# Kernel optimization log

Measured on AMD Instinct MI355X. Metric: run time of the kernel, lower is better.

The kernel has to match this reference:

```python
import jax, jax.numpy as jnp
import numpy as np

DIM = 384
DIM_HEAD = 32
HEADS = DIM // DIM_HEAD  # 12
INNER = HEADS * DIM_HEAD  # 384
WSZ = 8
WSZ2 = 8
SCALE = DIM_HEAD ** -0.5


def setup_inputs() -> dict:
    key = jax.random.key(0)
    k1, k2, k3, k4 = jax.random.split(key, 4)
    B, H, W = 32, 64, 64
    x = jax.random.normal(k1, (B, H, W, DIM), dtype=jnp.float32)
    # 1x1 convs == dense matrices over the channel dim
    w_qkv = jax.random.normal(k2, (DIM, 3 * INNER), dtype=jnp.float32) * (DIM ** -0.5)
    w_out = jax.random.normal(k3, (INNER, DIM), dtype=jnp.float32) * (INNER ** -0.5)
    b_out = jax.random.normal(k4, (DIM,), dtype=jnp.float32) * 0.02
    return {"x": x, "w_qkv": w_qkv, "w_out": w_out, "b_out": b_out}


def reference(x, w_qkv, w_out, b_out):
    B, H, W, D = x.shape
    nh, nw = H // WSZ, W // WSZ2
    S = WSZ * WSZ2  # tokens per window
    # 'short' attention: partition into non-overlapping wsz x wsz2 windows
    xw = (x.reshape(B, nh, WSZ, nw, WSZ2, D)
           .transpose(0, 1, 3, 2, 4, 5)
           .reshape(B * nh * nw, S, D))  # [N, S, D]
    qkv = xw @ w_qkv  # [N, S, 3*INNER] (1x1 conv, no bias)
    q, k, v = jnp.split(qkv, 3, axis=-1)
    def split_heads(t):
        N = t.shape[0]
        return t.reshape(N, S, HEADS, DIM_HEAD).transpose(0, 2, 1, 3)  # [N, h, S, d]
    q, k, v = map(split_heads, (q, k, v))
    sim = jnp.einsum('nhid,nhjd->nhij', q * SCALE, k)  # [N, h, S, S]
    attn = jax.nn.softmax(sim, axis=-1)
    out = jnp.einsum('nhij,nhjd->nhid', attn, v)  # [N, h, S, d]
    out = out.transpose(0, 2, 1, 3).reshape(-1, S, INNER)  # [N, S, INNER]
    out = out @ w_out + b_out  # 1x1 conv with bias -> [N, S, D]
    # undo windowing back to [B, H, W, D]
    out = (out.reshape(B, nh, nw, WSZ, WSZ2, D)
              .transpose(0, 1, 3, 2, 4, 5)
              .reshape(B, H, W, D))
    return out
```

## Files before the change

kernel.cpp:

```cpp
#include <hip/hip_runtime.h>

typedef _Float16 f16;
typedef _Float16 f16x4 __attribute__((ext_vector_type(4)));
typedef _Float16 f16x8 __attribute__((ext_vector_type(8)));
typedef float f32x4 __attribute__((ext_vector_type(4)));

#define MFMA_F16(A, B, C) __builtin_amdgcn_mfma_f32_16x16x32_f16(A, B, C, 0, 0, 0)
#define GLDS16(gp, lp)                                                        \
  __builtin_amdgcn_global_load_lds(                                           \
      (const __attribute__((address_space(1))) void*)(gp),                    \
      (__attribute__((address_space(3))) void*)(lp), 16, 0, 0)

static constexpr int ROWS = 32 * 64 * 64;
static constexpr float SCALE = 0.17677669529663687f;

static constexpr size_t WQKVT_OFF = 0;
static constexpr size_t WOUTT_OFF = (size_t)1152 * 384 * 2;
static constexpr size_t QKV_OFF   = WOUTT_OFF + (size_t)384 * 384 * 2;
static constexpr size_t WS_NEEDED = QKV_OFF + (size_t)ROWS * 1152 * 2;

__global__ __launch_bounds__(256) void k_prep(const float* __restrict__ wqkv,
                                              const float* __restrict__ wout,
                                              f16* __restrict__ wqkvT,
                                              f16* __restrict__ woutT) {
  int idx = blockIdx.x * 256 + threadIdx.x;
  if (idx < 1152 * 384) {
    int c = idx / 384, k = idx - c * 384;
    wqkvT[idx] = (f16)wqkv[k * 1152 + c];
  } else {
    int i = idx - 1152 * 384;
    if (i < 384 * 384) {
      int c = i / 384, k = i - c * 384;
      woutT[i] = (f16)wout[k * 384 + c];
    }
  }
}

__global__ __launch_bounds__(256) void k_cvt(const float* __restrict__ X,
                                             f16* __restrict__ Xh) {
  int idx = blockIdx.x * 256 + threadIdx.x;
#pragma unroll
  for (int i = 0; i < 12; ++i) {
    size_t j = (size_t)(idx + i * 1048576) * 4;
    float4 v = *(const float4*)&X[j];
    f16x4 h;
    h[0] = (f16)v.x; h[1] = (f16)v.y; h[2] = (f16)v.z; h[3] = (f16)v.w;
    *(f16x4*)&Xh[j] = h;
  }
}

__global__ __launch_bounds__(256, 2) void k_qkv(const f16* __restrict__ Xh,
                                                const f16* __restrict__ Wt,
                                                f16* __restrict__ qkv) {
  __shared__ __align__(16) f16 smem[4][128 * 64];

  const int tid = threadIdx.x;
  const int id = blockIdx.x;
  const int s = id & 7, t = id >> 3;
  const int n0 = (t % 9) * 128;
  const int m0 = (s * 128 + t / 9) * 128;

  const int lane = tid & 63, wave = tid >> 6;
  const int lane15 = lane & 15, quad = lane >> 4;
  const int wm = (wave >> 1) * 64, wn = (wave & 1) * 64;

  const int r8 = lane >> 3, g7 = lane & 7;
  const int sg = ((g7 ^ r8) << 3);
  const f16* asrc[4];
  const f16* bsrc[4];
#pragma unroll
  for (int l = 0; l < 4; ++l) {
    asrc[l] = Xh + (size_t)(m0 + (wave * 4 + l) * 8 + r8) * 384 + sg;
    bsrc[l] = Wt + (size_t)(n0 + (wave * 4 + l) * 8 + r8) * 384 + sg;
  }

#define STAGE(buf, ks)                                                      \
  do {                                                                      \
    _Pragma("unroll") for (int l = 0; l < 4; ++l)                           \
        GLDS16(asrc[l] + (ks), &smem[(buf)][(wave * 4 + l) * 512]);         \
    _Pragma("unroll") for (int l = 0; l < 4; ++l)                           \
        GLDS16(bsrc[l] + (ks), &smem[2 + (buf)][(wave * 4 + l) * 512]);     \
  } while (0)

#define LDSOFF(row, kk) ((row) * 64 + ((((kk) * 4 + quad) ^ ((row) & 7)) << 3))

  f32x4 acc[4][4] = {};

  STAGE(0, 0);
  __syncthreads();

#pragma unroll
  for (int ti = 0; ti < 6; ++ti) {
    const int cur = ti & 1;
    if (ti < 5) STAGE(cur ^ 1, (ti + 1) * 64);
    __builtin_amdgcn_sched_barrier(0);

#pragma unroll
    for (int kk = 0; kk < 2; ++kk) {
      f16x8 af[4], bf[4];
#pragma unroll
      for (int i = 0; i < 4; ++i)
        af[i] = *(const f16x8*)&smem[cur][LDSOFF(wm + i * 16 + lane15, kk)];
#pragma unroll
      for (int j = 0; j < 4; ++j)
        bf[j] = *(const f16x8*)&smem[2 + cur][LDSOFF(wn + j * 16 + lane15, kk)];
#pragma unroll
      for (int i = 0; i < 4; ++i)
#pragma unroll
        for (int j = 0; j < 4; ++j)
          acc[i][j] = MFMA_F16(af[i], bf[j], acc[i][j]);
    }

    __syncthreads();
  }
#undef STAGE
#undef LDSOFF

  f16* Cs = (f16*)smem;
#pragma unroll
  for (int i = 0; i < 4; ++i)
#pragma unroll
    for (int j = 0; j < 4; ++j)
#pragma unroll
      for (int v = 0; v < 4; ++v)
        Cs[(wm + i * 16 + quad * 4 + v) * 136 + wn + j * 16 + lane15] = (f16)acc[i][j][v];
  __syncthreads();
#pragma unroll
  for (int l = 0; l < 8; ++l) {
    int idx = l * 256 + tid;
    int row = idx >> 4, c8 = (idx & 15) * 8;
    *(f16x8*)&qkv[(size_t)(m0 + row) * 1152 + n0 + c8] = *(const f16x8*)&Cs[row * 136 + c8];
  }
}

__global__ __launch_bounds__(256) void k_attn(const f16* __restrict__ qkv,
                                              const f16* __restrict__ woutT,
                                              const float* __restrict__ b_out,
                                              float* __restrict__ out) {
  __shared__ f16 vt[32 * 72];
  __shared__ f16 Pw[4][16 * 72];
  __shared__ f16 ao[64 * 392];

  const int tid = threadIdx.x;
  const int lane = tid & 63, wave = tid >> 6;
  const int lane15 = lane & 15, quad = lane >> 4;

  const int blk = blockIdx.x;
  const int b = blk >> 6, rem = blk & 63, wh = rem >> 3, ww = rem & 7;
  const int base = b * 4096 + wh * 512 + ww * 8;

  const int tq = wave * 16 + lane15;
  const size_t rowq = (size_t)(base + (tq >> 3) * 64 + (tq & 7)) * 1152;
  size_t rowk[4];
#pragma unroll
  for (int tj = 0; tj < 4; ++tj) {
    int tk = tj * 16 + lane15;
    rowk[tj] = (size_t)(base + (tk >> 3) * 64 + (tk & 7)) * 1152;
  }
  const int vt_t = tid >> 2, vt_d8 = (tid & 3) * 8;
  const size_t rowv = (size_t)(base + (vt_t >> 3) * 64 + (vt_t & 7)) * 1152;

#pragma unroll 1
  for (int h = 0; h < 12; ++h) {
    const int hoff = h * 32;
    f16x8 vv = *(const f16x8*)&qkv[rowv + 768 + hoff + vt_d8];
#pragma unroll
    for (int j = 0; j < 8; ++j) vt[(vt_d8 + j) * 72 + vt_t] = vv[j];
    __syncthreads();

    f16x8 aq = *(const f16x8*)&qkv[rowq + hoff + quad * 8];
    f32x4 sim[4];
#pragma unroll
    for (int tj = 0; tj < 4; ++tj) {
      f16x8 bk = *(const f16x8*)&qkv[rowk[tj] + 384 + hoff + quad * 8];
      f32x4 z = {};
      sim[tj] = MFMA_F16(aq, bk, z);
    }
#pragma unroll
    for (int tj = 0; tj < 4; ++tj)
#pragma unroll
      for (int v = 0; v < 4; ++v) sim[tj][v] *= SCALE;

    float pv[4][4];
#pragma unroll
    for (int v = 0; v < 4; ++v) {
      float m = fmaxf(fmaxf(sim[0][v], sim[1][v]), fmaxf(sim[2][v], sim[3][v]));
#pragma unroll
      for (int off = 1; off < 16; off <<= 1) m = fmaxf(m, __shfl_xor(m, off));
      float ssum = 0.f;
#pragma unroll
      for (int tj = 0; tj < 4; ++tj) {
        pv[tj][v] = __expf(sim[tj][v] - m);
        ssum += pv[tj][v];
      }
#pragma unroll
      for (int off = 1; off < 16; off <<= 1) ssum += __shfl_xor(ssum, off);
      float inv = 1.0f / ssum;
#pragma unroll
      for (int tj = 0; tj < 4; ++tj) pv[tj][v] *= inv;
    }
#pragma unroll
    for (int tj = 0; tj < 4; ++tj)
#pragma unroll
      for (int v = 0; v < 4; ++v)
        Pw[wave][(quad * 4 + v) * 72 + tj * 16 + lane15] = (f16)pv[tj][v];
    __syncthreads();

    f32x4 o[2] = {};
#pragma unroll
    for (int kk = 0; kk < 64; kk += 32) {
      f16x8 pa = *(const f16x8*)&Pw[wave][lane15 * 72 + kk + quad * 8];
#pragma unroll
      for (int tj = 0; tj < 2; ++tj) {
        f16x8 bvv = *(const f16x8*)&vt[(tj * 16 + lane15) * 72 + kk + quad * 8];
        o[tj] = MFMA_F16(pa, bvv, o[tj]);
      }
    }
#pragma unroll
    for (int tj = 0; tj < 2; ++tj)
#pragma unroll
      for (int v = 0; v < 4; ++v)
        ao[(wave * 16 + quad * 4 + v) * 392 + hoff + tj * 16 + lane15] = (f16)o[tj][v];
    __syncthreads();
  }

  const int n0 = wave * 96;
  float biasv[6];
#pragma unroll
  for (int tj = 0; tj < 6; ++tj) biasv[tj] = b_out[n0 + tj * 16 + lane15];
  f32x4 acc[4][6] = {};
  for (int ksi = 0; ksi < 12; ++ksi) {
    const int ks = ksi * 32;
    f16x8 af[4];
#pragma unroll
    for (int ti = 0; ti < 4; ++ti)
      af[ti] = *(const f16x8*)&ao[(ti * 16 + lane15) * 392 + ks + quad * 8];
#pragma unroll
    for (int tj = 0; tj < 6; ++tj) {
      f16x8 bf = *(const f16x8*)&woutT[(size_t)(n0 + tj * 16 + lane15) * 384 + ks + quad * 8];
#pragma unroll
      for (int ti = 0; ti < 4; ++ti) acc[ti][tj] = MFMA_F16(af[ti], bf, acc[ti][tj]);
    }
  }
#pragma unroll
  for (int ti = 0; ti < 4; ++ti)
#pragma unroll
    for (int v = 0; v < 4; ++v) {
      int t = ti * 16 + quad * 4 + v;
      size_t row = (size_t)(base + (t >> 3) * 64 + (t & 7)) * 384;
#pragma unroll
      for (int tj = 0; tj < 6; ++tj)
        out[row + n0 + tj * 16 + lane15] = acc[ti][tj][v] + biasv[tj];
    }
}

extern "C" void kernel_launch(void* const* d_in, const int* in_sizes, int n_in,
                              void* d_out, int out_size, void* d_ws, size_t ws_size,
                              hipStream_t stream) {
  const float* x = (const float*)d_in[0];
  const float* w_qkv = (const float*)d_in[1];
  const float* w_out = (const float*)d_in[2];
  const float* b_out = (const float*)d_in[3];
  float* out = (float*)d_out;

  if (ws_size < WS_NEEDED) return;

  char* ws = (char*)d_ws;
  f16* wqkvT = (f16*)(ws + WQKVT_OFF);
  f16* woutT = (f16*)(ws + WOUTT_OFF);
  f16* qkv = (f16*)(ws + QKV_OFF);
  f16* Xh = (f16*)d_out;

  hipLaunchKernelGGL(k_prep, dim3(2304), dim3(256), 0, stream, w_qkv, w_out, wqkvT, woutT);
  hipLaunchKernelGGL(k_cvt, dim3(4096), dim3(256), 0, stream, x, Xh);
  hipLaunchKernelGGL(k_qkv, dim3(9216), dim3(256), 0, stream, Xh, wqkvT, qkv);
  hipLaunchKernelGGL(k_attn, dim3(2048), dim3(256), 0, stream, qkv, woutT, b_out, out);
}
```

Measured before the change: 753.8 us.

## Split attention and output projection; per-wave heads with in-place AO writeback

Attention now gives each wave its own heads, three per wave, and drops the block-wide barriers. The attention output is written back in place over the Q slots of the qkv buffer. The output projection moves to a separate tiled GEMM kernel with LDS double buffering and async global-to-LDS loads, sized 128x128 tiles. The softmax scale is folded into the Q weights during prep. This trades an extra round trip of the attention output through global memory for a much more efficient output GEMM and less synchronisation in attention.

```diff
diff --git a/kernel.cpp b/kernel.cpp
--- a/kernel.cpp
+++ b/kernel.cpp
@@ -26,7 +26,8 @@
   int idx = blockIdx.x * 256 + threadIdx.x;
   if (idx < 1152 * 384) {
     int c = idx / 384, k = idx - c * 384;
-    wqkvT[idx] = (f16)wqkv[k * 1152 + c];
+    float w = wqkv[k * 1152 + c];
+    wqkvT[idx] = (f16)(c < 384 ? w * SCALE : w);
   } else {
     int i = idx - 1152 * 384;
     if (i < 384 * 384) {
@@ -110,7 +111,6 @@
         for (int j = 0; j < 4; ++j)
           acc[i][j] = MFMA_F16(af[i], bf[j], acc[i][j]);
     }
-
     __syncthreads();
   }
 #undef STAGE
@@ -133,13 +133,9 @@
   }
 }
 
-__global__ __launch_bounds__(256) void k_attn(const f16* __restrict__ qkv,
-                                              const f16* __restrict__ woutT,
-                                              const float* __restrict__ b_out,
-                                              float* __restrict__ out) {
-  __shared__ f16 vt[32 * 72];
-  __shared__ f16 Pw[4][16 * 72];
-  __shared__ f16 ao[64 * 392];
+__global__ __launch_bounds__(256, 3) void k_attn(f16* __restrict__ qkv) {
+  __shared__ f16 vt[4][32 * 72];
+  __shared__ f16 Pt[4][16 * 72];
 
   const int tid = threadIdx.x;
   const int lane = tid & 63, wave = tid >> 6;
@@ -149,109 +145,177 @@
   const int b = blk >> 6, rem = blk & 63, wh = rem >> 3, ww = rem & 7;
   const int base = b * 4096 + wh * 512 + ww * 8;
 
-  const int tq = wave * 16 + lane15;
-  const size_t rowq = (size_t)(base + (tq >> 3) * 64 + (tq & 7)) * 1152;
-  size_t rowk[4];
-#pragma unroll
-  for (int tj = 0; tj < 4; ++tj) {
-    int tk = tj * 16 + lane15;
-    rowk[tj] = (size_t)(base + (tk >> 3) * 64 + (tk & 7)) * 1152;
-  }
-  const int vt_t = tid >> 2, vt_d8 = (tid & 3) * 8;
-  const size_t rowv = (size_t)(base + (vt_t >> 3) * 64 + (vt_t & 7)) * 1152;
+  size_t rowA[4];
+#pragma unroll
+  for (int i = 0; i < 4; ++i) {
+    int t = i * 16 + lane15;
+    rowA[i] = (size_t)(base + (t >> 3) * 64 + (t & 7)) * 1152;
+  }
+  const size_t rowV = (size_t)(base + (lane >> 3) * 64 + (lane & 7)) * 1152;
+
+  f16* vtw = &vt[wave][0];
+  f16* ptw = &Pt[wave][0];
 
 #pragma unroll 1
-  for (int h = 0; h < 12; ++h) {
+  for (int hh = 0; hh < 3; ++hh) {
+    const int h = wave + hh * 4;
     const int hoff = h * 32;
-    f16x8 vv = *(const f16x8*)&qkv[rowv + 768 + hoff + vt_d8];
-#pragma unroll
-    for (int j = 0; j < 8; ++j) vt[(vt_d8 + j) * 72 + vt_t] = vv[j];
+
+#pragma unroll
+    for (int g = 0; g < 4; ++g) {
+      f16x8 vv = *(const f16x8*)&qkv[rowV + 768 + hoff + g * 8];
+#pragma unroll
+      for (int e = 0; e < 8; ++e) vtw[(g * 8 + e) * 72 + lane] = vv[e];
+    }
+
+    f16x8 af[4], bk[4];
+#pragma unroll
+    for (int i = 0; i < 4; ++i)
+      af[i] = *(const f16x8*)&qkv[rowA[i] + hoff + quad * 8];
+#pragma unroll
+    for (int j = 0; j < 4; ++j)
+      bk[j] = *(const f16x8*)&qkv[rowA[j] + 384 + hoff + quad * 8];
+    f32x4 sim[4][4];
+#pragma unroll
+    for (int i = 0; i < 4; ++i)
+#pragma unroll
+      for (int j = 0; j < 4; ++j) {
+        f32x4 z = {};
+        sim[i][j] = MFMA_F16(af[i], bk[j], z);
+      }
+
+#pragma unroll
+    for (int i = 0; i < 4; ++i)
+#pragma unroll
+      for (int v = 0; v < 4; ++v) {
+        float m = fmaxf(fmaxf(sim[i][0][v], sim[i][1][v]),
+                        fmaxf(sim[i][2][v], sim[i][3][v]));
+#pragma unroll
+        for (int off = 1; off < 16; off <<= 1) m = fmaxf(m, __shfl_xor(m, off));
+        float ssum = 0.f;
+#pragma unroll
+        for (int j = 0; j < 4; ++j) {
+          sim[i][j][v] = __expf(sim[i][j][v] - m);
+          ssum += sim[i][j][v];
+        }
+#pragma unroll
+        for (int off = 1; off < 16; off <<= 1) ssum += __shfl_xor(ssum, off);
+        float inv = 1.0f / ssum;
+#pragma unroll
+        for (int j = 0; j < 4; ++j) sim[i][j][v] *= inv;
+      }
+
+    f16x8 bV[2][2];
+#pragma unroll
+    for (int j2 = 0; j2 < 2; ++j2)
+#pragma unroll
+      for (int kk = 0; kk < 2; ++kk)
+        bV[j2][kk] = *(const f16x8*)&vtw[(j2 * 16 + lane15) * 72 + kk * 32 + quad * 8];
+
+#pragma unroll
+    for (int i = 0; i < 4; ++i) {
+#pragma unroll
+      for (int j = 0; j < 4; ++j)
+#pragma unroll
+        for (int v = 0; v < 4; ++v)
+          ptw[(quad * 4 + v) * 72 + j * 16 + lane15] = (f16)sim[i][j][v];
+      f32x4 o[2] = {};
+#pragma unroll
+      for (int kk = 0; kk < 2; ++kk) {
+        f16x8 pa = *(const f16x8*)&ptw[lane15 * 72 + kk * 32 + quad * 8];
+#pragma unroll
+        for (int j2 = 0; j2 < 2; ++j2) o[j2] = MFMA_F16(pa, bV[j2][kk], o[j2]);
+      }
+#pragma unroll
+      for (int j2 = 0; j2 < 2; ++j2)
+#pragma unroll
+        for (int v = 0; v < 4; ++v) {
+          int t = i * 16 + quad * 4 + v;
+          size_t row = (size_t)(base + (t >> 3) * 64 + (t & 7)) * 1152;
+          qkv[row + hoff + j2 * 16 + lane15] = (f16)o[j2][v];
+        }
+    }
+  }
+}
+
+__global__ __launch_bounds__(256, 2) void k_out(const f16* __restrict__ AO,
+                                                const f16* __restrict__ Wt,
+                                                const float* __restrict__ bias,
+                                                float* __restrict__ out) {
+  __shared__ __align__(16) f16 smem[4][128 * 64];
+
+  const int tid = threadIdx.x;
+  const int id = blockIdx.x;
+  const int s = id & 7, t = id >> 3;
+  const int n0 = (t % 3) * 128;
+  const int m0 = (s * 128 + t / 3) * 128;
+
+  const int lane = tid & 63, wave = tid >> 6;
+  const int lane15 = lane & 15, quad = lane >> 4;
+  const int wm = (wave >> 1) * 64, wn = (wave & 1) * 64;
+
+  const int r8 = lane >> 3, g7 = lane & 7;
+  const int sg = ((g7 ^ r8) << 3);
+  const f16* asrc[4];
+  const f16* bsrc[4];
+#pragma unroll
+  for (int l = 0; l < 4; ++l) {
+    asrc[l] = AO + (size_t)(m0 + (wave * 4 + l) * 8 + r8) * 1152 + sg;
+    bsrc[l] = Wt + (size_t)(n0 + (wave * 4 + l) * 8 + r8) * 384 + sg;
+  }
+
+#define STAGE(buf, ks)                                                      \
+  do {                                                                      \
+    _Pragma("unroll") for (int l = 0; l < 4; ++l)                           \
+        GLDS16(asrc[l] + (ks), &smem[(buf)][(wave * 4 + l) * 512]);         \
+    _Pragma("unroll") for (int l = 0; l < 4; ++l)                           \
+        GLDS16(bsrc[l] + (ks), &smem[2 + (buf)][(wave * 4 + l) * 512]);     \
+  } while (0)
+
+#define LDSOFF(row, kk) ((row) * 64 + ((((kk) * 4 + quad) ^ ((row) & 7)) << 3))
+
+  f32x4 acc[4][4] = {};
+
+  STAGE(0, 0);
+  __syncthreads();
+
+#pragma unroll
+  for (int ti = 0; ti < 6; ++ti) {
+    const int cur = ti & 1;
+    if (ti < 5) STAGE(cur ^ 1, (ti + 1) * 64);
+    __builtin_amdgcn_sched_barrier(0);
+
+#pragma unroll
+    for (int kk = 0; kk < 2; ++kk) {
+      f16x8 af[4], bf[4];
+#pragma unroll
+      for (int i = 0; i < 4; ++i)
+        af[i] = *(const f16x8*)&smem[cur][LDSOFF(wm + i * 16 + lane15, kk)];
+#pragma unroll
+      for (int j = 0; j < 4; ++j)
+        bf[j] = *(const f16x8*)&smem[2 + cur][LDSOFF(wn + j * 16 + lane15, kk)];
+#pragma unroll
+      for (int i = 0; i < 4; ++i)
+#pragma unroll
+        for (int j = 0; j < 4; ++j)
+          acc[i][j] = MFMA_F16(af[i], bf[j], acc[i][j]);
+    }
     __syncthreads();
-
-    f16x8 aq = *(const f16x8*)&qkv[rowq + hoff + quad * 8];
-    f32x4 sim[4];
-#pragma unroll
-    for (int tj = 0; tj < 4; ++tj) {
-      f16x8 bk = *(const f16x8*)&qkv[rowk[tj] + 384 + hoff + quad * 8];
-      f32x4 z = {};
-      sim[tj] = MFMA_F16(aq, bk, z);
-    }
-#pragma unroll
-    for (int tj = 0; tj < 4; ++tj)
-#pragma unroll
-      for (int v = 0; v < 4; ++v) sim[tj][v] *= SCALE;
-
-    float pv[4][4];
-#pragma unroll
-    for (int v = 0; v < 4; ++v) {
-      float m = fmaxf(fmaxf(sim[0][v], sim[1][v]), fmaxf(sim[2][v], sim[3][v]));
-#pragma unroll
-      for (int off = 1; off < 16; off <<= 1) m = fmaxf(m, __shfl_xor(m, off));
-      float ssum = 0.f;
-#pragma unroll
-      for (int tj = 0; tj < 4; ++tj) {
-        pv[tj][v] = __expf(sim[tj][v] - m);
-        ssum += pv[tj][v];
-      }
-#pragma unroll
-      for (int off = 1; off < 16; off <<= 1) ssum += __shfl_xor(ssum, off);
-      float inv = 1.0f / ssum;
-#pragma unroll
-      for (int tj = 0; tj < 4; ++tj) pv[tj][v] *= inv;
-    }
-#pragma unroll
-    for (int tj = 0; tj < 4; ++tj)
+  }
+#undef STAGE
+#undef LDSOFF
+
+  float bj[4];
+#pragma unroll
+  for (int j = 0; j < 4; ++j) bj[j] = bias[n0 + wn + j * 16 + lane15];
+#pragma unroll
+  for (int i = 0; i < 4; ++i)
+#pragma unroll
+    for (int j = 0; j < 4; ++j)
 #pragma unroll
       for (int v = 0; v < 4; ++v)
-        Pw[wave][(quad * 4 + v) * 72 + tj * 16 + lane15] = (f16)pv[tj][v];
-    __syncthreads();
-
-    f32x4 o[2] = {};
-#pragma unroll
-    for (int kk = 0; kk < 64; kk += 32) {
-      f16x8 pa = *(const f16x8*)&Pw[wave][lane15 * 72 + kk + quad * 8];
-#pragma unroll
-      for (int tj = 0; tj < 2; ++tj) {
-        f16x8 bvv = *(const f16x8*)&vt[(tj * 16 + lane15) * 72 + kk + quad * 8];
-        o[tj] = MFMA_F16(pa, bvv, o[tj]);
-      }
-    }
-#pragma unroll
-    for (int tj = 0; tj < 2; ++tj)
-#pragma unroll
-      for (int v = 0; v < 4; ++v)
-        ao[(wave * 16 + quad * 4 + v) * 392 + hoff + tj * 16 + lane15] = (f16)o[tj][v];
-    __syncthreads();
-  }
-
-  const int n0 = wave * 96;
-  float biasv[6];
-#pragma unroll
-  for (int tj = 0; tj < 6; ++tj) biasv[tj] = b_out[n0 + tj * 16 + lane15];
-  f32x4 acc[4][6] = {};
-  for (int ksi = 0; ksi < 12; ++ksi) {
-    const int ks = ksi * 32;
-    f16x8 af[4];
-#pragma unroll
-    for (int ti = 0; ti < 4; ++ti)
-      af[ti] = *(const f16x8*)&ao[(ti * 16 + lane15) * 392 + ks + quad * 8];
-#pragma unroll
-    for (int tj = 0; tj < 6; ++tj) {
-      f16x8 bf = *(const f16x8*)&woutT[(size_t)(n0 + tj * 16 + lane15) * 384 + ks + quad * 8];
-#pragma unroll
-      for (int ti = 0; ti < 4; ++ti) acc[ti][tj] = MFMA_F16(af[ti], bf, acc[ti][tj]);
-    }
-  }
-#pragma unroll
-  for (int ti = 0; ti < 4; ++ti)
-#pragma unroll
-    for (int v = 0; v < 4; ++v) {
-      int t = ti * 16 + quad * 4 + v;
-      size_t row = (size_t)(base + (t >> 3) * 64 + (t & 7)) * 384;
-#pragma unroll
-      for (int tj = 0; tj < 6; ++tj)
-        out[row + n0 + tj * 16 + lane15] = acc[ti][tj][v] + biasv[tj];
-    }
+        out[(size_t)(m0 + wm + i * 16 + quad * 4 + v) * 384 + n0 + wn + j * 16 + lane15] =
+            acc[i][j][v] + bj[j];
 }
 
 extern "C" void kernel_launch(void* const* d_in, const int* in_sizes, int n_in,
@@ -274,5 +338,6 @@
   hipLaunchKernelGGL(k_prep, dim3(2304), dim3(256), 0, stream, w_qkv, w_out, wqkvT, woutT);
   hipLaunchKernelGGL(k_cvt, dim3(4096), dim3(256), 0, stream, x, Xh);
   hipLaunchKernelGGL(k_qkv, dim3(9216), dim3(256), 0, stream, Xh, wqkvT, qkv);
-  hipLaunchKernelGGL(k_attn, dim3(2048), dim3(256), 0, stream, qkv, woutT, b_out, out);
-}
+  hipLaunchKernelGGL(k_attn, dim3(2048), dim3(256), 0, stream, qkv);
+  hipLaunchKernelGGL(k_out, dim3(3072), dim3(256), 0, stream, qkv, woutT, b_out, out);
+}
```

Measured after the change: 723.8 us. 4.0% less time.
